# Performance work log

Hardware: AMD Instinct MI355X
Metric: run time of the kernel (lower is better)

Reference implementation:

```python
import jax, jax.numpy as jnp
import numpy as np

DIM = 512; HEADS = 8; DH = 64; B = 4; NL = 1024; NQ = 4096; VOCAB = 4096; MULT = 4
T_MIN = 1e-4; T_MAX = 2.0627; EPS = 1e-5


def _inv_freq():
    # POYO rotary: only first half of (head_dim//2) freq slots are nonzero (rotate_dim = head_dim//2)
    inv = np.zeros(DH // 2, dtype=np.float32)
    inv[: DH // 4] = (2.0 * np.pi / T_MIN) * (T_MIN / T_MAX) ** (
        np.arange(0, DH // 2, 2, dtype=np.float32) / (DH // 2))
    return jnp.asarray(inv)

INV_FREQ = _inv_freq()


def rotary_freqs(t):
    # t: (b, n) -> (b, n, DH), each freq repeated twice (interleaved pairs)
    return jnp.repeat(t[..., None] * INV_FREQ, 2, axis=-1)


def rotate_half(x):
    # interleaved pairs: (x0, x1) -> (-x1, x0)
    xp = x.reshape(x.shape[:-1] + (-1, 2))
    return jnp.stack((-xp[..., 1], xp[..., 0]), axis=-1).reshape(x.shape)


def apply_rot(freqs, x):
    # freqs: (b, n, DH); x: (b, n, h, DH)
    f = freqs[:, :, None, :]
    return x * jnp.cos(f) + rotate_half(x) * jnp.sin(f)


def layer_norm(x, w, b):
    mu = x.mean(-1, keepdims=True)
    var = x.var(-1, keepdims=True)
    return (x - mu) * jax.lax.rsqrt(var + EPS) * w + b


def setup_inputs() -> dict:
    key = jax.random.key(0)
    ks = jax.random.split(key, 16)
    lin = lambda k, fi, shp: (jax.random.normal(k, shp, jnp.float32) / np.sqrt(fi)).astype(jnp.float32)
    inner = HEADS * DH
    hid = DIM * MULT
    return {
        'encoder_latents': jax.random.normal(ks[0], (B, NL, DIM), jnp.float32),
        'latent_timestamps': jax.random.uniform(ks[1], (B, NL), jnp.float32, 0.0, 2.0),
        'query_unit_index': jax.random.randint(ks[2], (B, NQ), 0, VOCAB),
        'query_timestamps': jax.random.uniform(ks[3], (B, NQ), jnp.float32, 0.0, 2.0),
        'unit_emb': 0.02 * jax.random.normal(ks[4], (VOCAB, DIM // 2), jnp.float32),
        'vp_w': jnp.zeros((DIM // 2, 1), jnp.float32),
        'vp_b': jnp.zeros((DIM // 2,), jnp.float32),
        'ca_norm_w': jnp.ones((DIM,), jnp.float32), 'ca_norm_b': jnp.zeros((DIM,), jnp.float32),
        'ca_ctx_w': jnp.ones((DIM,), jnp.float32), 'ca_ctx_b': jnp.zeros((DIM,), jnp.float32),
        'wq': lin(ks[5], DIM, (inner, DIM)),
        'wkv': lin(ks[6], DIM, (2 * inner, DIM)),
        'wo': lin(ks[7], inner, (DIM, inner)), 'bo': jnp.zeros((DIM,), jnp.float32),
        'ffn_ln_w': jnp.ones((DIM,), jnp.float32), 'ffn_ln_b': jnp.zeros((DIM,), jnp.float32),
        'w1': lin(ks[8], DIM, (2 * hid, DIM)), 'b1': jnp.zeros((2 * hid,), jnp.float32),
        'w2': lin(ks[9], hid, (DIM, hid)), 'b2': jnp.zeros((DIM,), jnp.float32),
        'out_ln_w': jnp.ones((DIM,), jnp.float32), 'out_ln_b': jnp.zeros((DIM,), jnp.float32),
        'wproj': lin(ks[10], DIM, (1, DIM)), 'bproj': jnp.zeros((1,), jnp.float32),
    }


def reference(encoder_latents, latent_timestamps, query_unit_index, query_timestamps,
              unit_emb, vp_w, vp_b, ca_norm_w, ca_norm_b, ca_ctx_w, ca_ctx_b,
              wq, wkv, wo, bo, ffn_ln_w, ffn_ln_b, w1, b1, w2, b2,
              out_ln_w, out_ln_b, wproj, bproj):
    b, nq = query_unit_index.shape
    inner = HEADS * DH
    # query tokens: zero dummy values -> Linear(1, dim//2) reduces to its bias; concat with unit embedding
    qv = jnp.broadcast_to(vp_b + 0.0 * vp_w.sum(), (b, nq, DIM // 2))
    qtok = jnp.concatenate([qv, unit_emb[query_unit_index]], axis=-1)  # (b, nq, DIM)
    qpos = rotary_freqs(query_timestamps)      # (b, nq, DH)
    lpos = rotary_freqs(latent_timestamps)     # (b, nl, DH)
    # rotary cross-attention (rotate_value=True)
    xn = layer_norm(qtok, ca_norm_w, ca_norm_b)
    cn = layer_norm(encoder_latents, ca_ctx_w, ca_ctx_b)
    q = (xn @ wq.T).reshape(b, nq, HEADS, DH)
    kv = cn @ wkv.T
    k = kv[..., :inner].reshape(b, -1, HEADS, DH)
    v = kv[..., inner:].reshape(b, -1, HEADS, DH)
    q = apply_rot(qpos, q)
    k = apply_rot(lpos, k)
    v = apply_rot(lpos, v)
    scores = jnp.einsum('bqhd,bkhd->bhqk', q, k) * (DH ** -0.5)
    attn = jax.nn.softmax(scores, axis=-1)
    out = jnp.einsum('bhqk,bkhd->bqhd', attn, v)
    out = apply_rot(-qpos, out)               # un-rotate values back to query frame
    out = out.reshape(b, nq, inner) @ wo.T + bo
    dec = qtok + out
    # GEGLU FFN with pre-LayerNorm
    h = layer_norm(dec, ffn_ln_w, ffn_ln_b) @ w1.T + b1
    a, g = jnp.split(h, 2, axis=-1)
    dec = dec + (a * jax.nn.gelu(g, approximate=False)) @ w2.T + b2
    dec = layer_norm(dec, out_ln_w, out_ln_b)
    return dec @ wproj.T + bproj              # (b, nq, 1)
```

## Files before the change

### kernel.cpp

```cpp
#include <hip/hip_runtime.h>
#include <math.h>


typedef unsigned short u16;
typedef __attribute__((ext_vector_type(8))) short bf16x8;
typedef __attribute__((ext_vector_type(4))) float f32x4;

__device__ __forceinline__ u16 f2b(float x) {
    union { float f; unsigned u; } v; v.f = x;
    unsigned r = v.u + 0x7fffu + ((v.u >> 16) & 1u);
    return (u16)(r >> 16);
}
__device__ __forceinline__ float b2f(u16 h) {
    union { unsigned u; float f; } v; v.u = ((unsigned)h) << 16;
    return v.f;
}
__device__ __forceinline__ f32x4 mfma32(bf16x8 a, bf16x8 b, f32x4 c) {
    return __builtin_amdgcn_mfma_f32_16x16x32_bf16(a, b, c, 0, 0, 0);
}
__device__ __forceinline__ void gl16(const u16* g, u16* l) {
    __builtin_amdgcn_global_load_lds((const __attribute__((address_space(1))) void*)g,
                                     (__attribute__((address_space(3))) void*)l,
                                     16, 0, 0);
}

__global__ __launch_bounds__(256) void k_cvt(const float* __restrict__ in,
                                             u16* __restrict__ out, const int n)
{
    const int i = (blockIdx.x * 256 + threadIdx.x) * 4;
    if (i >= n) return;
    const float4 v = *(const float4*)&in[i];
    ushort4 o;
    o.x = f2b(v.x); o.y = f2b(v.y); o.z = f2b(v.z); o.w = f2b(v.w);
    *(ushort4*)&out[i] = o;
}

__global__ void k_rope_tab16(const float* __restrict__ t, float* __restrict__ tab,
                             const int n)
{
    const int idx = blockIdx.x * 256 + threadIdx.x;
    if (idx >= n * 16) return;
    const int r = idx >> 4, i = idx & 15;
    const float b0 = (float)(1e-4 / 2.0627);
    const float a0 = (float)(2.0 * 3.14159265358979323846 / 1e-4);
    const float invf = a0 * (float)pow((double)b0, (double)i * (1.0 / 16.0));
    const float ang = t[r] * invf;
    float sn, cs;
    sincosf(ang, &sn, &cs);
    tab[((size_t)r << 5) + (i << 1)]     = cs;
    tab[((size_t)r << 5) + (i << 1) + 1] = sn;
}

__global__ __launch_bounds__(128) void k_qtok_ln(
    const int* __restrict__ qidx, const float* __restrict__ uemb,
    const float* __restrict__ vpb, const float* __restrict__ w,
    const float* __restrict__ bb, u16* __restrict__ qtok, u16* __restrict__ xn)
{
    const int r = blockIdx.x, tid = threadIdx.x, c0 = tid << 2;
    float4 x;
    if (c0 < 256) {
        x = *(const float4*)&vpb[c0];
    } else {
        const int u = qidx[r];
        x = *(const float4*)&uemb[(size_t)u * 256 + (c0 - 256)];
    }
    ushort4 qo;
    qo.x = f2b(x.x); qo.y = f2b(x.y); qo.z = f2b(x.z); qo.w = f2b(x.w);
    *(ushort4*)&qtok[(size_t)r * 512 + c0] = qo;
    float s  = x.x + x.y + x.z + x.w;
    float s2 = x.x * x.x + x.y * x.y + x.z * x.z + x.w * x.w;
#pragma unroll
    for (int o = 32; o > 0; o >>= 1) { s += __shfl_down(s, o); s2 += __shfl_down(s2, o); }
    __shared__ float buf[4];
    if ((tid & 63) == 0) { buf[(tid >> 6) << 1] = s; buf[((tid >> 6) << 1) + 1] = s2; }
    __syncthreads();
    s = buf[0] + buf[2]; s2 = buf[1] + buf[3];
    const float mu = s * (1.f / 512.f);
    const float rs = rsqrtf(s2 * (1.f / 512.f) - mu * mu + 1e-5f);
    const float4 w4 = *(const float4*)&w[c0];
    const float4 b4 = *(const float4*)&bb[c0];
    ushort4 yo;
    yo.x = f2b((x.x - mu) * rs * w4.x + b4.x);
    yo.y = f2b((x.y - mu) * rs * w4.y + b4.y);
    yo.z = f2b((x.z - mu) * rs * w4.z + b4.z);
    yo.w = f2b((x.w - mu) * rs * w4.w + b4.w);
    *(ushort4*)&xn[(size_t)r * 512 + c0] = yo;
}

__global__ __launch_bounds__(128) void k_ln_f(
    const float* __restrict__ in, const float* __restrict__ w,
    const float* __restrict__ bb, u16* __restrict__ outp)
{
    const int r = blockIdx.x, tid = threadIdx.x, c0 = tid << 2;
    const float4 x = *(const float4*)&in[(size_t)r * 512 + c0];
    float s  = x.x + x.y + x.z + x.w;
    float s2 = x.x * x.x + x.y * x.y + x.z * x.z + x.w * x.w;
#pragma unroll
    for (int o = 32; o > 0; o >>= 1) { s += __shfl_down(s, o); s2 += __shfl_down(s2, o); }
    __shared__ float buf[4];
    if ((tid & 63) == 0) { buf[(tid >> 6) << 1] = s; buf[((tid >> 6) << 1) + 1] = s2; }
    __syncthreads();
    s = buf[0] + buf[2]; s2 = buf[1] + buf[3];
    const float mu = s * (1.f / 512.f);
    const float rs = rsqrtf(s2 * (1.f / 512.f) - mu * mu + 1e-5f);
    const float4 w4 = *(const float4*)&w[c0];
    const float4 b4 = *(const float4*)&bb[c0];
    ushort4 yo;
    yo.x = f2b((x.x - mu) * rs * w4.x + b4.x);
    yo.y = f2b((x.y - mu) * rs * w4.y + b4.y);
    yo.z = f2b((x.z - mu) * rs * w4.z + b4.z);
    yo.w = f2b((x.w - mu) * rs * w4.w + b4.w);
    *(ushort4*)&outp[(size_t)r * 512 + c0] = yo;
}

__global__ __launch_bounds__(128) void k_ln_h(
    const u16* __restrict__ in, const float* __restrict__ w,
    const float* __restrict__ bb, u16* __restrict__ outp)
{
    const int r = blockIdx.x, tid = threadIdx.x, c0 = tid << 2;
    const ushort4 xi = *(const ushort4*)&in[(size_t)r * 512 + c0];
    float4 x;
    x.x = b2f(xi.x); x.y = b2f(xi.y); x.z = b2f(xi.z); x.w = b2f(xi.w);
    float s  = x.x + x.y + x.z + x.w;
    float s2 = x.x * x.x + x.y * x.y + x.z * x.z + x.w * x.w;
#pragma unroll
    for (int o = 32; o > 0; o >>= 1) { s += __shfl_down(s, o); s2 += __shfl_down(s2, o); }
    __shared__ float buf[4];
    if ((tid & 63) == 0) { buf[(tid >> 6) << 1] = s; buf[((tid >> 6) << 1) + 1] = s2; }
    __syncthreads();
    s = buf[0] + buf[2]; s2 = buf[1] + buf[3];
    const float mu = s * (1.f / 512.f);
    const float rs = rsqrtf(s2 * (1.f / 512.f) - mu * mu + 1e-5f);
    const float4 w4 = *(const float4*)&w[c0];
    const float4 b4 = *(const float4*)&bb[c0];
    ushort4 yo;
    yo.x = f2b((x.x - mu) * rs * w4.x + b4.x);
    yo.y = f2b((x.y - mu) * rs * w4.y + b4.y);
    yo.z = f2b((x.z - mu) * rs * w4.z + b4.z);
    yo.w = f2b((x.w - mu) * rs * w4.w + b4.w);
    *(ushort4*)&outp[(size_t)r * 512 + c0] = yo;
}

template <int EPI>
__global__ __launch_bounds__(256) void k_mgemm(
    const u16* __restrict__ A, const u16* __restrict__ W,
    const int N, const int K,
    u16* __restrict__ out0, u16* __restrict__ out1,
    const float* __restrict__ bias, const u16* __restrict__ res,
    const float* __restrict__ tab)
{
    __shared__ u16 Al[128 * 32];
    __shared__ u16 Bl[128 * 32];
    const int bm = blockIdx.y << 7, bn = blockIdx.x << 7;
    const int tid = threadIdx.x;
    const int w = tid >> 6, l = tid & 63;
    const int wm = w >> 1, wn = w & 1;
    const int lr = l & 15, hi = l >> 4;
    const int srow = l >> 2, skq = (l & 3) << 3;
    const u16* Ap0 = A + (size_t)(bm + 16 * w + srow) * K + skq;
    const u16* Ap1 = A + (size_t)(bm + 64 + 16 * w + srow) * K + skq;
    const u16* Wp0 = W + (size_t)(bn + 16 * w + srow) * K + skq;
    const u16* Wp1 = W + (size_t)(bn + 64 + 16 * w + srow) * K + skq;
    u16* lA0 = Al + 512 * w;
    u16* lA1 = Al + 2048 + 512 * w;
    u16* lB0 = Bl + 512 * w;
    u16* lB1 = Bl + 2048 + 512 * w;
    f32x4 acc[4][4];
#pragma unroll
    for (int i = 0; i < 4; i++)
#pragma unroll
        for (int j = 0; j < 4; j++)
#pragma unroll
            for (int e = 0; e < 4; e++) acc[i][j][e] = 0.f;
    for (int k0 = 0; k0 < K; k0 += 32) {
        __syncthreads();
        gl16(Ap0 + k0, lA0);
        gl16(Ap1 + k0, lA1);
        gl16(Wp0 + k0, lB0);
        gl16(Wp1 + k0, lB1);
        __syncthreads();
        bf16x8 av[4], bv[4];
#pragma unroll
        for (int mi = 0; mi < 4; mi++)
            av[mi] = *(const bf16x8*)&Al[(wm * 64 + mi * 16 + lr) * 32 + hi * 8];
#pragma unroll
        for (int nj = 0; nj < 4; nj++)
            bv[nj] = *(const bf16x8*)&Bl[(wn * 64 + nj * 16 + lr) * 32 + hi * 8];
#pragma unroll
        for (int mi = 0; mi < 4; mi++)
#pragma unroll
            for (int nj = 0; nj < 4; nj++)
                acc[mi][nj] = mfma32(av[mi], bv[nj], acc[mi][nj]);
    }
#pragma unroll
    for (int mi = 0; mi < 4; mi++) {
#pragma unroll
        for (int nj = 0; nj < 4; nj++) {
            const int c = bn + wn * 64 + nj * 16 + lr;
#pragma unroll
            for (int j = 0; j < 4; j++) {
                const int r = bm + wm * 64 + mi * 16 + hi * 4 + j;
                const float x = acc[mi][nj][j];
                if (EPI == 2) {
                    const float y = x + bias[c] + b2f(res[(size_t)r * 512 + c]);
                    out0[(size_t)r * 512 + c] = f2b(y);
                } else {
                    const float p = __shfl_xor(x, 1);
                    const int ci = c & 63;
                    float y = x;
                    if (ci < 32) {
                        const int ii = ci >> 1;
                        const float cc = tab[((size_t)r << 5) + (ii << 1)];
                        const float ss = tab[((size_t)r << 5) + (ii << 1) + 1];
                        y = (c & 1) ? fmaf(x, cc, p * ss) : fmaf(x, cc, -p * ss);
                    }
                    if (EPI == 0) {
                        out0[(size_t)r * 512 + c] = f2b(y);
                    } else {
                        if (c < 512) {
                            out0[(size_t)r * 512 + c] = f2b(y * 0.125f);
                        } else {
                            const int d = c - 512, hh = d >> 6, dd = d & 63;
                            const int bq = r >> 10, pos = r & 1023;
                            out1[(((size_t)(bq * 8 + hh)) * 64 + dd) * 1024 + pos] = f2b(y);
                        }
                    }
                }
            }
        }
    }
}

__global__ __launch_bounds__(256) void k_mffn1(
    const u16* __restrict__ A, const u16* __restrict__ W1,
    const float* __restrict__ b1, u16* __restrict__ ag)
{
    __shared__ u16 Al[128 * 32];
    __shared__ u16 Bl[128 * 32];
    const int bm = blockIdx.y << 7, bn = blockIdx.x << 6;
    const int tid = threadIdx.x;
    const int w = tid >> 6, l = tid & 63;
    const int wm = w >> 1, wn = w & 1;
    const int lr = l & 15, hi = l >> 4;
    const int srow = l >> 2, skq = (l & 3) << 3;
    const u16* Ap0 = A  + (size_t)(bm + 16 * w + srow) * 512 + skq;
    const u16* Ap1 = A  + (size_t)(bm + 64 + 16 * w + srow) * 512 + skq;
    const u16* Wa  = W1 + (size_t)(bn + 16 * w + srow) * 512 + skq;
    const u16* Wg  = W1 + (size_t)(2048 + bn + 16 * w + srow) * 512 + skq;
    u16* lA0 = Al + 512 * w;
    u16* lA1 = Al + 2048 + 512 * w;
    u16* lB0 = Bl + 512 * w;
    u16* lB1 = Bl + 2048 + 512 * w;
    f32x4 acca[4][2], accg[4][2];
#pragma unroll
    for (int i = 0; i < 4; i++)
#pragma unroll
        for (int j = 0; j < 2; j++)
#pragma unroll
            for (int e = 0; e < 4; e++) { acca[i][j][e] = 0.f; accg[i][j][e] = 0.f; }
    for (int k0 = 0; k0 < 512; k0 += 32) {
        __syncthreads();
        gl16(Ap0 + k0, lA0);
        gl16(Ap1 + k0, lA1);
        gl16(Wa + k0, lB0);
        gl16(Wg + k0, lB1);
        __syncthreads();
        bf16x8 av[4], ba[2], bg[2];
#pragma unroll
        for (int mi = 0; mi < 4; mi++)
            av[mi] = *(const bf16x8*)&Al[(wm * 64 + mi * 16 + lr) * 32 + hi * 8];
#pragma unroll
        for (int nj = 0; nj < 2; nj++) {
            ba[nj] = *(const bf16x8*)&Bl[(wn * 32 + nj * 16 + lr) * 32 + hi * 8];
            bg[nj] = *(const bf16x8*)&Bl[(wn * 32 + nj * 16 + lr + 64) * 32 + hi * 8];
        }
#pragma unroll
        for (int mi = 0; mi < 4; mi++)
#pragma unroll
            for (int nj = 0; nj < 2; nj++) {
                acca[mi][nj] = mfma32(av[mi], ba[nj], acca[mi][nj]);
                accg[mi][nj] = mfma32(av[mi], bg[nj], accg[mi][nj]);
            }
    }
#pragma unroll
    for (int mi = 0; mi < 4; mi++)
#pragma unroll
        for (int nj = 0; nj < 2; nj++) {
            const int c = bn + wn * 32 + nj * 16 + lr;
#pragma unroll
            for (int j = 0; j < 4; j++) {
                const int r = bm + wm * 64 + mi * 16 + hi * 4 + j;
                const float a = acca[mi][nj][j] + b1[c];
                const float g = accg[mi][nj][j] + b1[2048 + c];
                const float ge = 0.5f * g * (1.f + erff(g * 0.70710678118654752f));
                ag[(size_t)r * 2048 + c] = f2b(a * ge);
            }
        }
}

__global__ __launch_bounds__(256) void k_mattn(
    const u16* __restrict__ q, const u16* __restrict__ kbuf,
    const u16* __restrict__ vT, const float* __restrict__ tab,
    u16* __restrict__ ao, const int rowbase)
{
    const int bid = blockIdx.x, tid = threadIdx.x;
    const int h = bid & 7, qi = bid >> 3;
    const int qbase = qi << 7;
    const int w = tid >> 6, l = tid & 63;
    const int lr = l & 15, hi = l >> 4;
    const int qrA = qbase + w * 32 + lr;
    const int qrB = qrA + 16;
    const int b = (rowbase + qbase) >> 12;
    const bf16x8 qfA0 = *(const bf16x8*)&q[(size_t)qrA * 512 + h * 64 + hi * 8];
    const bf16x8 qfA1 = *(const bf16x8*)&q[(size_t)qrA * 512 + h * 64 + hi * 8 + 32];
    const bf16x8 qfB0 = *(const bf16x8*)&q[(size_t)qrB * 512 + h * 64 + hi * 8];
    const bf16x8 qfB1 = *(const bf16x8*)&q[(size_t)qrB * 512 + h * 64 + hi * 8 + 32];
    const u16* Kp = kbuf + (size_t)b * 524288 + h * 64;
    const u16* Vp = vT + ((size_t)(b * 8 + h)) * 65536;
    const int g2 = (hi & 1) * 2;
    const int srcA = lr + (g2 << 4);
    const int srcB = srcA + 16;
    const bool up = (hi >> 1) != 0;
    f32x4 accA[4], accB[4];
#pragma unroll
    for (int dj = 0; dj < 4; dj++)
#pragma unroll
        for (int e = 0; e < 4; e++) { accA[dj][e] = 0.f; accB[dj][e] = 0.f; }
    float mA = -1e30f, lA = 0.f, mB = -1e30f, lB = 0.f;
    for (int kc = 0; kc < 1024; kc += 64) {
        f32x4 stA[4], stB[4];
#pragma unroll
        for (int t = 0; t < 4; t++) {
            const size_t krow = (size_t)(kc + t * 16 + lr) * 512 + hi * 8;
            const bf16x8 kf0 = *(const bf16x8*)&Kp[krow];
            const bf16x8 kf1 = *(const bf16x8*)&Kp[krow + 32];
#pragma unroll
            for (int e = 0; e < 4; e++) { stA[t][e] = 0.f; stB[t][e] = 0.f; }
            stA[t] = mfma32(kf0, qfA0, stA[t]);
            stA[t] = mfma32(kf1, qfA1, stA[t]);
            stB[t] = mfma32(kf0, qfB0, stB[t]);
            stB[t] = mfma32(kf1, qfB1, stB[t]);
        }
        bf16x8 pfragA[2], pfragB[2];
        {
            float mx = -1e30f;
#pragma unroll
            for (int t = 0; t < 4; t++)
#pragma unroll
                for (int j = 0; j < 4; j++) mx = fmaxf(mx, stA[t][j]);
            mx = fmaxf(mx, __shfl_xor(mx, 16));
            mx = fmaxf(mx, __shfl_xor(mx, 32));
            if (!__all(mx - mA <= 8.f)) {
                const float mnew = fmaxf(mA, mx);
                const float alpha = __expf(mA - mnew);
                lA *= alpha;
#pragma unroll
                for (int dj = 0; dj < 4; dj++)
#pragma unroll
                    for (int e = 0; e < 4; e++) accA[dj][e] *= alpha;
                mA = mnew;
            }
            float ps = 0.f;
            unsigned P64[4][2];
#pragma unroll
            for (int t = 0; t < 4; t++) {
                const float p0 = __expf(stA[t][0] - mA);
                const float p1 = __expf(stA[t][1] - mA);
                const float p2 = __expf(stA[t][2] - mA);
                const float p3 = __expf(stA[t][3] - mA);
                ps += (p0 + p1) + (p2 + p3);
                P64[t][0] = (unsigned)f2b(p0) | ((unsigned)f2b(p1) << 16);
                P64[t][1] = (unsigned)f2b(p2) | ((unsigned)f2b(p3) << 16);
            }
            ps += __shfl_xor(ps, 16);
            ps += __shfl_xor(ps, 32);
            lA += ps;
#pragma unroll
            for (int ks = 0; ks < 2; ks++) {
                const unsigned c0x = P64[ks * 2 + 0][0], c0y = P64[ks * 2 + 0][1];
                const unsigned c1x = P64[ks * 2 + 1][0], c1y = P64[ks * 2 + 1][1];
                const unsigned a0x = (unsigned)__shfl((int)c0x, srcA);
                const unsigned a0y = (unsigned)__shfl((int)c0y, srcA);
                const unsigned a1x = (unsigned)__shfl((int)c1x, srcA);
                const unsigned a1y = (unsigned)__shfl((int)c1y, srcA);
                const unsigned b0x = (unsigned)__shfl((int)c0x, srcB);
                const unsigned b0y = (unsigned)__shfl((int)c0y, srcB);
                const unsigned b1x = (unsigned)__shfl((int)c1x, srcB);
                const unsigned b1y = (unsigned)__shfl((int)c1y, srcB);
                union { unsigned u[4]; bf16x8 v; } pk;
                pk.u[0] = up ? a1x : a0x;
                pk.u[1] = up ? a1y : a0y;
                pk.u[2] = up ? b1x : b0x;
                pk.u[3] = up ? b1y : b0y;
                pfragA[ks] = pk.v;
            }
        }
        {
            float mx = -1e30f;
#pragma unroll
            for (int t = 0; t < 4; t++)
#pragma unroll
                for (int j = 0; j < 4; j++) mx = fmaxf(mx, stB[t][j]);
            mx = fmaxf(mx, __shfl_xor(mx, 16));
            mx = fmaxf(mx, __shfl_xor(mx, 32));
            if (!__all(mx - mB <= 8.f)) {
                const float mnew = fmaxf(mB, mx);
                const float alpha = __expf(mB - mnew);
                lB *= alpha;
#pragma unroll
                for (int dj = 0; dj < 4; dj++)
#pragma unroll
                    for (int e = 0; e < 4; e++) accB[dj][e] *= alpha;
                mB = mnew;
            }
            float ps = 0.f;
            unsigned P64[4][2];
#pragma unroll
            for (int t = 0; t < 4; t++) {
                const float p0 = __expf(stB[t][0] - mB);
                const float p1 = __expf(stB[t][1] - mB);
                const float p2 = __expf(stB[t][2] - mB);
                const float p3 = __expf(stB[t][3] - mB);
                ps += (p0 + p1) + (p2 + p3);
                P64[t][0] = (unsigned)f2b(p0) | ((unsigned)f2b(p1) << 16);
                P64[t][1] = (unsigned)f2b(p2) | ((unsigned)f2b(p3) << 16);
            }
            ps += __shfl_xor(ps, 16);
            ps += __shfl_xor(ps, 32);
            lB += ps;
#pragma unroll
            for (int ks = 0; ks < 2; ks++) {
                const unsigned c0x = P64[ks * 2 + 0][0], c0y = P64[ks * 2 + 0][1];
                const unsigned c1x = P64[ks * 2 + 1][0], c1y = P64[ks * 2 + 1][1];
                const unsigned a0x = (unsigned)__shfl((int)c0x, srcA);
                const unsigned a0y = (unsigned)__shfl((int)c0y, srcA);
                const unsigned a1x = (unsigned)__shfl((int)c1x, srcA);
                const unsigned a1y = (unsigned)__shfl((int)c1y, srcA);
                const unsigned b0x = (unsigned)__shfl((int)c0x, srcB);
                const unsigned b0y = (unsigned)__shfl((int)c0y, srcB);
                const unsigned b1x = (unsigned)__shfl((int)c1x, srcB);
                const unsigned b1y = (unsigned)__shfl((int)c1y, srcB);
                union { unsigned u[4]; bf16x8 v; } pk;
                pk.u[0] = up ? a1x : a0x;
                pk.u[1] = up ? a1y : a0y;
                pk.u[2] = up ? b1x : b0x;
                pk.u[3] = up ? b1y : b0y;
                pfragB[ks] = pk.v;
            }
        }
#pragma unroll
        for (int dj = 0; dj < 4; dj++)
#pragma unroll
            for (int ks = 0; ks < 2; ks++) {
                const bf16x8 vf = *(const bf16x8*)
                    &Vp[(size_t)(dj * 16 + lr) * 1024 + kc + ks * 32 + hi * 8];
                accA[dj] = mfma32(vf, pfragA[ks], accA[dj]);
                accB[dj] = mfma32(vf, pfragB[ks], accB[dj]);
            }
    }
    const float ivA = 1.f / lA, ivB = 1.f / lB;
#pragma unroll
    for (int g = 0; g < 2; g++) {
        const int qr = g ? qrB : qrA;
        const float invl = g ? ivB : ivA;
#pragma unroll
        for (int dj = 0; dj < 4; dj++) {
            const f32x4 a = g ? accB[dj] : accA[dj];
            const int d0 = dj * 16 + hi * 4;
            float y[4];
#pragma unroll
            for (int pp = 0; pp < 2; pp++) {
                const float x0 = a[2 * pp] * invl;
                const float x1 = a[2 * pp + 1] * invl;
                const int ii = (d0 >> 1) + pp;
                if (ii < 16) {
                    const float cc = tab[((size_t)qr << 5) + (ii << 1)];
                    const float ss = tab[((size_t)qr << 5) + (ii << 1) + 1];
                    y[2 * pp]     = fmaf(x0, cc, x1 * ss);
                    y[2 * pp + 1] = fmaf(x1, cc, -x0 * ss);
                } else {
                    y[2 * pp] = x0; y[2 * pp + 1] = x1;
                }
            }
            ushort4 o;
            o.x = f2b(y[0]); o.y = f2b(y[1]); o.z = f2b(y[2]); o.w = f2b(y[3]);
            *(ushort4*)&ao[(size_t)qr * 512 + h * 64 + d0] = o;
        }
    }
}

__global__ __launch_bounds__(128) void k_final(
    const u16* __restrict__ dec, const float* __restrict__ w,
    const float* __restrict__ bb, const float* __restrict__ wproj,
    const float* __restrict__ bproj, float* __restrict__ out)
{
    const int r = blockIdx.x, tid = threadIdx.x, c0 = tid << 2;
    const ushort4 xi = *(const ushort4*)&dec[(size_t)r * 512 + c0];
    float4 x;
    x.x = b2f(xi.x); x.y = b2f(xi.y); x.z = b2f(xi.z); x.w = b2f(xi.w);
    float s  = x.x + x.y + x.z + x.w;
    float s2 = x.x * x.x + x.y * x.y + x.z * x.z + x.w * x.w;
#pragma unroll
    for (int o = 32; o > 0; o >>= 1) { s += __shfl_down(s, o); s2 += __shfl_down(s2, o); }
    __shared__ float buf[4];
    if ((tid & 63) == 0) { buf[(tid >> 6) << 1] = s; buf[((tid >> 6) << 1) + 1] = s2; }
    __syncthreads();
    s = buf[0] + buf[2]; s2 = buf[1] + buf[3];
    const float mu = s * (1.f / 512.f);
    const float rs = rsqrtf(s2 * (1.f / 512.f) - mu * mu + 1e-5f);
    const float4 w4 = *(const float4*)&w[c0];
    const float4 b4 = *(const float4*)&bb[c0];
    const float4 p4 = *(const float4*)&wproj[c0];
    float part = ((x.x - mu) * rs * w4.x + b4.x) * p4.x
               + ((x.y - mu) * rs * w4.y + b4.y) * p4.y
               + ((x.z - mu) * rs * w4.z + b4.z) * p4.z
               + ((x.w - mu) * rs * w4.w + b4.w) * p4.w;
#pragma unroll
    for (int o = 32; o > 0; o >>= 1) part += __shfl_down(part, o);
    __shared__ float buf2[2];
    if ((tid & 63) == 0) buf2[tid >> 6] = part;
    __syncthreads();
    if (tid == 0) out[r] = buf2[0] + buf2[1] + bproj[0];
}

extern "C" void kernel_launch(void* const* d_in, const int* in_sizes, int n_in,
                              void* d_out, int out_size, void* d_ws, size_t ws_size,
                              hipStream_t stream)
{
    (void)in_sizes; (void)n_in; (void)out_size;
    const float* enc  = (const float*)d_in[0];
    const float* lts  = (const float*)d_in[1];
    const int*   qidx = (const int*)  d_in[2];
    const float* qts  = (const float*)d_in[3];
    const float* uemb = (const float*)d_in[4];
    const float* vpb  = (const float*)d_in[6];
    const float* canw = (const float*)d_in[7];
    const float* canb = (const float*)d_in[8];
    const float* ccw  = (const float*)d_in[9];
    const float* ccb  = (const float*)d_in[10];
    const float* wq   = (const float*)d_in[11];
    const float* wkv  = (const float*)d_in[12];
    const float* wo   = (const float*)d_in[13];
    const float* bo   = (const float*)d_in[14];
    const float* flnw = (const float*)d_in[15];
    const float* flnb = (const float*)d_in[16];
    const float* w1   = (const float*)d_in[17];
    const float* b1   = (const float*)d_in[18];
    const float* w2   = (const float*)d_in[19];
    const float* b2   = (const float*)d_in[20];
    const float* olnw = (const float*)d_in[21];
    const float* olnb = (const float*)d_in[22];
    const float* wpj  = (const float*)d_in[23];
    const float* bpj  = (const float*)d_in[24];
    float* outp = (float*)d_out;

    float* tabq = (float*)d_ws;
    float* tabl = tabq + 524288;
    u16* wqb  = (u16*)(tabl + 131072);
    u16* wkvb = wqb + 262144;
    u16* wob  = wkvb + 524288;
    u16* w1b  = wob + 262144;
    u16* w2b  = w1b + 2097152;
    u16* cn   = w2b + 1048576;
    u16* kb   = cn + 2097152;
    u16* vT   = kb + 2097152;
    const size_t base_b = 2621440ull + 20971520ull;
    int CQ = 16384;
    while (CQ > 512 &&
           base_b + (size_t)CQ * 5120 + (size_t)(CQ < 4096 ? CQ : 4096) * 4096 > ws_size)
        CQ >>= 1;
    int SF = CQ;
    while (SF > 512 && base_b + (size_t)CQ * 5120 + (size_t)SF * 4096 > ws_size)
        SF >>= 1;
    u16* qtokC = vT + 2097152;
    u16* xnC   = qtokC + (size_t)CQ * 512;
    u16* qC    = xnC + (size_t)CQ * 512;
    u16* aoC   = qC + (size_t)CQ * 512;
    u16* d2C   = aoC + (size_t)CQ * 512;
    u16* agC   = d2C + (size_t)CQ * 512;

    k_cvt<<<256, 256, 0, stream>>>(wq, wqb, 262144);
    k_cvt<<<512, 256, 0, stream>>>(wkv, wkvb, 524288);
    k_cvt<<<256, 256, 0, stream>>>(wo, wob, 262144);
    k_cvt<<<2048, 256, 0, stream>>>(w1, w1b, 2097152);
    k_cvt<<<1024, 256, 0, stream>>>(w2, w2b, 1048576);
    k_rope_tab16<<<1024, 256, 0, stream>>>(qts, tabq, 16384);
    k_rope_tab16<<<256, 256, 0, stream>>>(lts, tabl, 4096);
    k_ln_f<<<4096, 128, 0, stream>>>(enc, ccw, ccb, cn);
    k_mgemm<1><<<dim3(8, 32), 256, 0, stream>>>(cn, wkvb, 1024, 512,
                                                kb, vT, nullptr, nullptr, tabl);

    for (int g0 = 0; g0 < 16384; g0 += CQ) {
        const float* tabc = tabq + (size_t)g0 * 32;
        k_qtok_ln<<<CQ, 128, 0, stream>>>(qidx + g0, uemb, vpb, canw, canb,
                                          qtokC, xnC);
        k_mgemm<0><<<dim3(4, CQ / 128), 256, 0, stream>>>(xnC, wqb, 512, 512,
                                                          qC, nullptr, nullptr, nullptr, tabc);
        k_mattn<<<(CQ / 128) * 8, 256, 0, stream>>>(qC, kb, vT, tabc, aoC, g0);
        k_mgemm<2><<<dim3(4, CQ / 128), 256, 0, stream>>>(aoC, wob, 512, 512,
                                                          d2C, nullptr, bo, qtokC, nullptr);
        k_ln_h<<<CQ, 128, 0, stream>>>(d2C, flnw, flnb, xnC);
        for (int f0 = 0; f0 < CQ; f0 += SF) {
            k_mffn1<<<dim3(32, SF / 128), 256, 0, stream>>>(xnC + (size_t)f0 * 512,
                                                            w1b, b1, agC);
            k_mgemm<2><<<dim3(4, SF / 128), 256, 0, stream>>>(agC, w2b, 512, 2048,
                                                              qC + (size_t)f0 * 512, nullptr,
                                                              b2, d2C + (size_t)f0 * 512, nullptr);
            k_final<<<SF, 128, 0, stream>>>(qC + (size_t)f0 * 512, olnw, olnb,
                                            wpj, bpj, outp + g0 + f0);
        }
    }
}
```

Measured before the change: 412.4 us.

## Split attention KV range across wave pairs and merge partial softmax via LDS

Each attention block now covers 64 queries instead of 128, and two waves share each 32-query group, each processing half of the 1024 keys. The partial max, sum and accumulators are combined through shared memory with a log-sum-exp merge, and the grid doubles to raise parallelism. V fragment loads are also hoisted ahead of the softmax to overlap memory latency. The cost is extra LDS traffic, a block-wide barrier, and idle half-waves during the epilogue.

```diff
diff --git a/kernel.cpp b/kernel.cpp
--- a/kernel.cpp
+++ b/kernel.cpp
@@ -303,12 +303,14 @@
     const u16* __restrict__ vT, const float* __restrict__ tab,
     u16* __restrict__ ao, const int rowbase)
 {
+    __shared__ float mrg[2][64][37];
     const int bid = blockIdx.x, tid = threadIdx.x;
     const int h = bid & 7, qi = bid >> 3;
-    const int qbase = qi << 7;
+    const int qbase = qi << 6;
     const int w = tid >> 6, l = tid & 63;
+    const int p = w >> 1, ko = (w & 1) << 9;
     const int lr = l & 15, hi = l >> 4;
-    const int qrA = qbase + w * 32 + lr;
+    const int qrA = qbase + p * 32 + lr;
     const int qrB = qrA + 16;
     const int b = (rowbase + qbase) >> 12;
     const bf16x8 qfA0 = *(const bf16x8*)&q[(size_t)qrA * 512 + h * 64 + hi * 8];
@@ -327,7 +329,8 @@
 #pragma unroll
         for (int e = 0; e < 4; e++) { accA[dj][e] = 0.f; accB[dj][e] = 0.f; }
     float mA = -1e30f, lA = 0.f, mB = -1e30f, lB = 0.f;
-    for (int kc = 0; kc < 1024; kc += 64) {
+    for (int kk = 0; kk < 512; kk += 64) {
+        const int kc = ko + kk;
         f32x4 stA[4], stB[4];
 #pragma unroll
         for (int t = 0; t < 4; t++) {
@@ -341,6 +344,13 @@
             stB[t] = mfma32(kf0, qfB0, stB[t]);
             stB[t] = mfma32(kf1, qfB1, stB[t]);
         }
+        bf16x8 vf[4][2];
+#pragma unroll
+        for (int dj = 0; dj < 4; dj++)
+#pragma unroll
+            for (int ks = 0; ks < 2; ks++)
+                vf[dj][ks] = *(const bf16x8*)
+                    &Vp[(size_t)(dj * 16 + lr) * 1024 + kc + ks * 32 + hi * 8];
         bf16x8 pfragA[2], pfragB[2];
         {
             float mx = -1e30f;
@@ -452,11 +462,46 @@
         for (int dj = 0; dj < 4; dj++)
 #pragma unroll
             for (int ks = 0; ks < 2; ks++) {
-                const bf16x8 vf = *(const bf16x8*)
-                    &Vp[(size_t)(dj * 16 + lr) * 1024 + kc + ks * 32 + hi * 8];
-                accA[dj] = mfma32(vf, pfragA[ks], accA[dj]);
-                accB[dj] = mfma32(vf, pfragB[ks], accB[dj]);
-            }
+                accA[dj] = mfma32(vf[dj][ks], pfragA[ks], accA[dj]);
+                accB[dj] = mfma32(vf[dj][ks], pfragB[ks], accB[dj]);
+            }
+    }
+    if (w & 1) {
+        float* dst = mrg[p][l];
+        dst[0] = mA; dst[1] = lA; dst[2] = mB; dst[3] = lB;
+#pragma unroll
+        for (int dj = 0; dj < 4; dj++)
+#pragma unroll
+            for (int e = 0; e < 4; e++) {
+                dst[4 + dj * 4 + e]  = accA[dj][e];
+                dst[20 + dj * 4 + e] = accB[dj][e];
+            }
+    }
+    __syncthreads();
+    if (w & 1) return;
+    {
+        const float* src = mrg[p][l];
+        const float m1A = src[0], l1A = src[1], m1B = src[2], l1B = src[3];
+        {
+            const float mm = fmaxf(mA, m1A);
+            const float f0 = __expf(mA - mm), f1 = __expf(m1A - mm);
+            lA = lA * f0 + l1A * f1;
+#pragma unroll
+            for (int dj = 0; dj < 4; dj++)
+#pragma unroll
+                for (int e = 0; e < 4; e++)
+                    accA[dj][e] = accA[dj][e] * f0 + src[4 + dj * 4 + e] * f1;
+        }
+        {
+            const float mm = fmaxf(mB, m1B);
+            const float f0 = __expf(mB - mm), f1 = __expf(m1B - mm);
+            lB = lB * f0 + l1B * f1;
+#pragma unroll
+            for (int dj = 0; dj < 4; dj++)
+#pragma unroll
+                for (int e = 0; e < 4; e++)
+                    accB[dj][e] = accB[dj][e] * f0 + src[20 + dj * 4 + e] * f1;
+        }
     }
     const float ivA = 1.f / lA, ivB = 1.f / lB;
 #pragma unroll
@@ -596,7 +641,7 @@
                                           qtokC, xnC);
         k_mgemm<0><<<dim3(4, CQ / 128), 256, 0, stream>>>(xnC, wqb, 512, 512,
                                                           qC, nullptr, nullptr, nullptr, tabc);
-        k_mattn<<<(CQ / 128) * 8, 256, 0, stream>>>(qC, kb, vT, tabc, aoC, g0);
+        k_mattn<<<(CQ / 64) * 8, 256, 0, stream>>>(qC, kb, vT, tabc, aoC, g0);
         k_mgemm<2><<<dim3(4, CQ / 128), 256, 0, stream>>>(aoC, wob, 512, 512,
                                                           d2C, nullptr, bo, qtokC, nullptr);
         k_ln_h<<<CQ, 128, 0, stream>>>(d2C, flnw, flnb, xnC);
```

Measured after the change: 409.9 us. Within noise of the previous version (-0.6%).
